# Kernel optimization log

Hardware: AMD Instinct MI355X
Metric: run time of the kernel (lower is better)

Reference implementation:

```python
import jax, jax.numpy as jnp
import numpy as np

B, N, E = 4, 2048, 1024          # batch, seq, embed_dim
H = 8                            # num_heads
D1 = 3 * E                       # expand_ratio * embed_dim = 3072 (already divisible by H)
DH = D1 // H                     # head_dim = 384
R = 512                          # rpe_embedding
GAMMA = 0.99
EPS = 1e-8


def _srms(x):
    # SimpleRMSNorm: x / (||x||_2 * d^{-1/2} + eps), no learned params
    rms = jnp.linalg.norm(x, axis=-1, keepdims=True) * (x.shape[-1] ** -0.5)
    return x / (rms + EPS)


def setup_inputs() -> dict:
    key = jax.random.key(0)
    ks = jax.random.split(key, 20)

    def lin(k, din, dout):
        kw, kb = jax.random.split(k)
        w = jax.random.normal(kw, (din, dout), jnp.float32) * (din ** -0.5)
        b = jax.random.normal(kb, (dout,), jnp.float32) * 0.02
        return w, b

    x = jax.random.normal(ks[0], (B, N, E), jnp.float32)
    u_w, u_b = lin(ks[1], E, D1)
    v_w, v_b = lin(ks[2], E, D1)
    o_w, o_b = lin(ks[3], D1, E)
    pos_w, pos_b = lin(ks[4], 1, R)
    lw0, lb0 = lin(ks[5], R, R)
    lw1, lb1 = lin(ks[6], R, R)
    lw2, lb2 = lin(ks[7], R, R)
    out_w, out_b = lin(ks[8], R, H * DH)
    return dict(x=x, u_w=u_w, u_b=u_b, v_w=v_w, v_b=v_b, o_w=o_w, o_b=o_b,
                pos_w=pos_w, pos_b=pos_b, lw0=lw0, lb0=lb0, lw1=lw1, lb1=lb1,
                lw2=lw2, lb2=lb2, out_w=out_w, out_b=out_b)


def reference(x, u_w, u_b, v_w, v_b, o_w, o_b,
              pos_w, pos_b, lw0, lb0, lw1, lb1, lw2, lb2, out_w, out_b):
    b, n, _ = x.shape
    # gated projections
    u = jax.nn.silu(x @ u_w + u_b)                       # (b, n, d1)
    v = jax.nn.silu(x @ v_w + v_b)                       # (b, n, d1)
    v = v.reshape(b, n, H, DH).transpose(0, 2, 1, 3)     # (b, h, n, d)

    # --- Tno: RPE MLP produces Toeplitz coefficients for lags 0..n-1 ---
    pos_idx = jnp.arange(n, dtype=x.dtype)[:, None]      # (n, 1)
    h_ = pos_idx @ pos_w + pos_b                         # (n, R)
    for w, bb in ((lw0, lb0), (lw1, lb1), (lw2, lb2)):
        h_ = jax.nn.relu(_srms(h_)) @ w + bb             # non-residual rpe layers
    coefs = jax.nn.relu(_srms(h_)) @ out_w + out_b       # (n, h*d)
    coefs = coefs.reshape(n, H, DH).transpose(1, 0, 2)   # (h, n, d)

    zero = coefs[:, :1]                                  # lag 0
    pos = coefs[:, 1:]                                   # lags 1..n-1
    decay = GAMMA ** jnp.arange(1, n, dtype=x.dtype)[None, :, None]
    pos = pos * decay                                    # use_decay with fixed gamma buffer
    # causal: negative lags are zero; cat([zero, pos, zero]) then zero-pad to 2n
    a = jnp.concatenate([zero, pos, zero], axis=1)       # (h, n+1, d)

    # circular conv of length 2n == causal Toeplitz matmul
    m = 2 * n
    av = jnp.fft.rfft(a, m, axis=1)                      # (h, m//2+1, d)
    xv = jnp.fft.rfft(v, m, axis=2)                      # (b, h, m//2+1, d)
    tv = jnp.fft.irfft(av[None] * xv, m, axis=2)[:, :, :n, :]

    out = tv.transpose(0, 2, 1, 3).reshape(b, n, H * DH) # (b, n, d1)
    out = u * out                                        # gate
    return out @ o_w + o_b                               # (b, n, e)
```

## Files before the change

### kernel.cpp

```cpp
#include <hip/hip_runtime.h>
#include <hip/hip_bf16.h>
#include <math.h>

#define GAMMA_ 0.99f
#define EPS_ 1e-8f

typedef __attribute__((ext_vector_type(8))) short s16x8;
typedef __attribute__((ext_vector_type(4))) float f32x4;
typedef __attribute__((address_space(1))) const ushort GASu;
typedef __attribute__((address_space(3))) ushort LASu;

__device__ __forceinline__ unsigned short f2bf(float f){
  unsigned u = __float_as_uint(f);
  unsigned r = (u + 0x7FFFu + ((u >> 16) & 1u)) >> 16;
  return (unsigned short)r;
}
__device__ __forceinline__ float bf2f(unsigned short h){
  return __uint_as_float(((unsigned)h) << 16);
}

__device__ __forceinline__ float2 cmul(float2 a, float2 b){
  return make_float2(a.x*b.x - a.y*b.y, a.x*b.y + a.y*b.x);
}
__device__ __forceinline__ float2 cadd(float2 a, float2 b){ return make_float2(a.x+b.x, a.y+b.y); }
__device__ __forceinline__ float2 csub(float2 a, float2 b){ return make_float2(a.x-b.x, a.y-b.y); }

__device__ void fft_dif(float2* z, const float2* tw, int tid){
  for (int s = 0; s < 12; ++s){
    __syncthreads();
    int half = 2048 >> s;
    for (int b = tid; b < 2048; b += 256){
      int j  = b & (half - 1);
      int g  = b >> (11 - s);
      int i0 = (g << (12 - s)) + j;
      int i1 = i0 + half;
      float2 u = z[i0], v = z[i1];
      z[i0] = cadd(u, v);
      z[i1] = cmul(csub(u, v), tw[j << s]);
    }
  }
  __syncthreads();
}
__device__ void fft_dit(float2* z, const float2* tw, int tid){
  for (int s = 0; s < 12; ++s){
    __syncthreads();
    int half = 1 << s;
    for (int b = tid; b < 2048; b += 256){
      int j  = b & (half - 1);
      int g  = b >> s;
      int i0 = (g << (s + 1)) + j;
      int i1 = i0 + half;
      float2 u = z[i0];
      float2 t = cmul(z[i1], tw[j << (11 - s)]);
      z[i0] = cadd(u, t);
      z[i1] = csub(u, t);
    }
  }
  __syncthreads();
}
__device__ __forceinline__ void tw_init(float2* tw, int tid){
  for (int j = tid; j < 2048; j += 256){
    float th = -(float)(3.14159265358979323846 / 2048.0) * (float)j;
    float s_, c_; __sincosf(th, &s_, &c_);
    tw[j] = make_float2(c_, s_);
  }
}
__device__ __forceinline__ int rev12(int x){ return (int)(__brev((unsigned)x) >> 20); }

__global__ __launch_bounds__(256)
void transpose_split(const float* __restrict__ W, ushort* __restrict__ Th,
                     ushort* __restrict__ Tl, int K, int N){
  __shared__ float T[32][33];
  int n0 = blockIdx.x * 32, k0 = blockIdx.y * 32;
  int tid = threadIdx.x;
  int j = tid & 31, i = tid >> 5;
#pragma unroll
  for (int p = 0; p < 4; ++p)
    T[i + 8*p][j] = W[(size_t)(k0 + i + 8*p) * N + n0 + j];
  __syncthreads();
#pragma unroll
  for (int p = 0; p < 4; ++p){
    int r = i + 8*p;
    float f = T[j][r];
    unsigned short hh = f2bf(f);
    Th[(size_t)(n0 + r) * K + k0 + j] = hh;
    Tl[(size_t)(n0 + r) * K + k0 + j] = f2bf(f - bf2f(hh));
  }
}

template<int ACT, int OUTMODE, int ASRC>
__global__ __launch_bounds__(256)
void gemm_mfma(const float* __restrict__ Af,
               const ushort* __restrict__ Ah, const ushort* __restrict__ Al,
               const ushort* __restrict__ Bh, const ushort* __restrict__ Bl,
               const float* __restrict__ bias,
               float* __restrict__ C, ushort* __restrict__ Ch, ushort* __restrict__ Cl,
               int M, int N, int K)
{
  __shared__ ushort Ash[128*32];
  __shared__ ushort Asl[128*32];
  __shared__ ushort Bsh[128*32];
  __shared__ ushort Bsl[128*32];
  int tid = threadIdx.x;
  int gx = gridDim.x;
  int nwg = gx * gridDim.y;
  int flat = blockIdx.y * gx + blockIdx.x;
  int s = (flat & 7) * (nwg >> 3) + (flat >> 3);
  int bx = s % gx, by = s / gx;
  int row0 = by * 128, col0 = bx * 128;
  int w = tid >> 6, lane = tid & 63;
  int wm = w >> 1, wn = w & 1;
  int lr = lane & 15, lg = lane >> 4;
  f32x4 acc[4][4] = {};

  for (int k0 = 0; k0 < K; k0 += 32){
    __syncthreads();
#pragma unroll
    for (int i = 0; i < 2; ++i){
      int p   = (w << 7) + (i << 6) + lane;
      int r   = p >> 2, chp = p & 3;
      int ch  = chp ^ ((r >> 1) & 3);
      int lbase = (w << 10) + (i << 9);
      size_t gb = (size_t)(col0 + r) * K + k0 + (ch << 3);
      __builtin_amdgcn_global_load_lds((GASu*)(Bh + gb), (LASu*)(Bsh + lbase), 16, 0, 0);
      __builtin_amdgcn_global_load_lds((GASu*)(Bl + gb), (LASu*)(Bsl + lbase), 16, 0, 0);
      if (ASRC == 0){
        size_t ga = (size_t)(row0 + r) * K + k0 + (ch << 3);
        __builtin_amdgcn_global_load_lds((GASu*)(Ah + ga), (LASu*)(Ash + lbase), 16, 0, 0);
        __builtin_amdgcn_global_load_lds((GASu*)(Al + ga), (LASu*)(Asl + lbase), 16, 0, 0);
      }
    }
    if (ASRC == 1){
#pragma unroll
      for (int pp = 0; pp < 2; ++pp){
        int c = tid + (pp << 8);
        int r = c >> 2, ch = c & 3;
        int kk = ch << 3;
        int off = (r << 5) + ((ch ^ ((r >> 1) & 3)) << 3);
        const float* src = &Af[(size_t)(row0 + r) * K + k0 + kk];
        float4 f0 = *(const float4*)src;
        float4 f1 = *(const float4*)(src + 4);
        float fs[8] = {f0.x, f0.y, f0.z, f0.w, f1.x, f1.y, f1.z, f1.w};
        uint hv[4], lv[4];
#pragma unroll
        for (int q = 0; q < 4; ++q){
          unsigned short h0 = f2bf(fs[2*q]),     h1 = f2bf(fs[2*q+1]);
          unsigned short l0 = f2bf(fs[2*q]   - bf2f(h0));
          unsigned short l1 = f2bf(fs[2*q+1] - bf2f(h1));
          hv[q] = (uint)h0 | ((uint)h1 << 16);
          lv[q] = (uint)l0 | ((uint)l1 << 16);
        }
        *(uint4*)&Ash[off] = make_uint4(hv[0], hv[1], hv[2], hv[3]);
        *(uint4*)&Asl[off] = make_uint4(lv[0], lv[1], lv[2], lv[3]);
      }
    }
    __syncthreads();
    s16x8 ah[4], al[4], bh[4], bl[4];
#pragma unroll
    for (int m = 0; m < 4; ++m){
      int row = wm*64 + m*16 + lr;
      int aoff = (row << 5) + ((lg ^ ((row >> 1) & 3)) << 3);
      ah[m] = *(const s16x8*)&Ash[aoff];
      al[m] = *(const s16x8*)&Asl[aoff];
    }
#pragma unroll
    for (int n = 0; n < 4; ++n){
      int row = wn*64 + n*16 + lr;
      int boff = (row << 5) + ((lg ^ ((row >> 1) & 3)) << 3);
      bh[n] = *(const s16x8*)&Bsh[boff];
      bl[n] = *(const s16x8*)&Bsl[boff];
    }
#pragma unroll
    for (int m = 0; m < 4; ++m)
#pragma unroll
      for (int n = 0; n < 4; ++n){
        acc[m][n] = __builtin_amdgcn_mfma_f32_16x16x32_bf16(ah[m], bh[n], acc[m][n], 0, 0, 0);
        acc[m][n] = __builtin_amdgcn_mfma_f32_16x16x32_bf16(ah[m], bl[n], acc[m][n], 0, 0, 0);
        acc[m][n] = __builtin_amdgcn_mfma_f32_16x16x32_bf16(al[m], bh[n], acc[m][n], 0, 0, 0);
      }
  }

#pragma unroll
  for (int m = 0; m < 4; ++m){
    int grow_base = row0 + wm*64 + m*16 + lg*4;
#pragma unroll
    for (int n = 0; n < 4; ++n){
      int gcol = col0 + wn*64 + n*16 + lr;
      float bv = bias[gcol];
      if (OUTMODE == 1){
        float4 o; float* op = (float*)&o;
#pragma unroll
        for (int r = 0; r < 4; ++r){
          float v2 = acc[m][n][r] + bv;
          if (ACT) v2 = v2 / (1.f + __expf(-v2));
          op[r] = v2;
        }
        int bb = grow_base >> 11, t = grow_base & 2047;
        *(float4*)&C[((size_t)bb * N + gcol) * 2048 + t] = o;
      } else {
#pragma unroll
        for (int r = 0; r < 4; ++r){
          float v2 = acc[m][n][r] + bv;
          if (ACT) v2 = v2 / (1.f + __expf(-v2));
          int grow = grow_base + r;
          if (OUTMODE == 0){
            C[(size_t)grow * N + gcol] = v2;
          } else {
            unsigned short hh = f2bf(v2);
            Ch[(size_t)grow * N + gcol] = hh;
            Cl[(size_t)grow * N + gcol] = f2bf(v2 - bf2f(hh));
          }
        }
      }
    }
  }
}

__global__ __launch_bounds__(256)
void pos_init(const float* __restrict__ pw, const float* __restrict__ pb, float* __restrict__ h){
  int idx = blockIdx.x * 256 + threadIdx.x;
  int t = idx >> 9, r = idx & 511;
  h[idx] = (float)t * pw[r] + pb[r];
}

__global__ __launch_bounds__(256)
void srms_relu_split(const float* __restrict__ in, ushort* __restrict__ oh,
                     ushort* __restrict__ ol){
  __shared__ float red[256];
  int row = blockIdx.x, tid = threadIdx.x;
  const float* r = in + (size_t)row * 512;
  float a = r[tid], b = r[tid + 256];
  red[tid] = a*a + b*b;
  __syncthreads();
  for (int off = 128; off > 0; off >>= 1){
    if (tid < off) red[tid] += red[tid + off];
    __syncthreads();
  }
  float rms = sqrtf(red[0] * (1.f / 512.f));
  float inv = 1.f / (rms + EPS_);
  size_t base = (size_t)row * 512;
  float va = a * inv; va = va > 0.f ? va : 0.f;
  float vb = b * inv; vb = vb > 0.f ? vb : 0.f;
  unsigned short ha = f2bf(va), hb = f2bf(vb);
  oh[base + tid]       = ha; ol[base + tid]       = f2bf(va - bf2f(ha));
  oh[base + tid + 256] = hb; ol[base + tid + 256] = f2bf(vb - bf2f(hb));
}

__global__ __launch_bounds__(256)
void build_aspec(const float* __restrict__ coefs_t, float2* __restrict__ aspec, int pbase){
  __shared__ float2 z[4096];
  __shared__ float2 tw[2048];
  int tid = threadIdx.x, slot = blockIdx.x, p = pbase + slot;
  tw_init(tw, tid);
  const float* c0 = coefs_t + (size_t)(2*p) * 2048;
  const float* c1 = c0 + 2048;
  const float l2g = log2f(GAMMA_);
  for (int t = tid; t < 2048; t += 256){
    float g = exp2f(l2g * (float)t);
    z[t] = make_float2(c0[t] * g, c1[t] * g);
  }
  for (int t = 2048 + tid; t < 4096; t += 256) z[t] = make_float2(0.f, 0.f);
  fft_dif(z, tw, tid);
  for (int k = tid; k <= 2048; k += 256){
    float2 zk = z[rev12(k)];
    float2 zm = z[rev12((4096 - k) & 4095)];
    float2 A0 = make_float2(0.5f*(zk.x + zm.x),  0.5f*(zk.y - zm.y));
    float2 A1 = make_float2(0.5f*(zk.y + zm.y), -0.5f*(zk.x - zm.x));
    *(float4*)(aspec + ((size_t)slot * 2049 + k) * 2) = make_float4(A0.x, A0.y, A1.x, A1.y);
  }
}

__global__ __launch_bounds__(256)
void conv_fft(float* __restrict__ vt, const float4* __restrict__ aspec, int pbase){
  __shared__ float2 z[4096];
  __shared__ float2 tw[2048];
  int tid = threadIdx.x, slot = blockIdx.x, p = pbase + slot, bb = blockIdx.y;
  tw_init(tw, tid);
  float* v0 = vt + ((size_t)bb * 3072 + 2*p) * 2048;
  float* v1 = v0 + 2048;
  for (int t = tid; t < 2048; t += 256) z[t] = make_float2(v0[t], v1[t]);
  for (int t = 2048 + tid; t < 4096; t += 256) z[t] = make_float2(0.f, 0.f);
  fft_dif(z, tw, tid);
  for (int k = tid; k <= 2048; k += 256){
    int rk  = rev12(k);
    int rmk = rev12((4096 - k) & 4095);
    float2 zk = z[rk], zm = z[rmk];
    float2 V0 = make_float2(0.5f*(zk.x + zm.x),  0.5f*(zk.y - zm.y));
    float2 V1 = make_float2(0.5f*(zk.y + zm.y), -0.5f*(zk.x - zm.x));
    float4 av = aspec[(size_t)slot * 2049 + k];
    float2 P0 = cmul(V0, make_float2(av.x, av.y));
    float2 P1 = cmul(V1, make_float2(av.z, av.w));
    z[rk]  = make_float2(P0.x - P1.y, -(P0.y + P1.x));
    z[rmk] = make_float2(P0.x + P1.y,   P0.y - P1.x);
  }
  fft_dit(z, tw, tid);
  const float sc = 1.f / 4096.f;
  for (int t = tid; t < 2048; t += 256){
    float2 w = z[t];
    v0[t] =  w.x * sc;
    v1[t] = -w.y * sc;
  }
}

__global__ __launch_bounds__(256)
void fuse_mul_inplace(ushort* uh, ushort* ul, const float* __restrict__ vt){
  __shared__ float T[64][65];
  int tid = threadIdx.x;
  int c0 = blockIdx.x * 64, t0 = blockIdx.y * 64;
  size_t b = blockIdx.z;
  {
    int j = tid >> 2, q = tid & 3;
    const float* src = vt + ((b * 3072 + c0 + j) * 2048 + t0 + q * 16);
#pragma unroll
    for (int f = 0; f < 4; ++f){
      float4 v = *(const float4*)(src + f * 4);
      T[j][q*16 + f*4 + 0] = v.x;
      T[j][q*16 + f*4 + 1] = v.y;
      T[j][q*16 + f*4 + 2] = v.z;
      T[j][q*16 + f*4 + 3] = v.w;
    }
  }
  __syncthreads();
  int i = tid >> 3, jq = tid & 7;
#pragma unroll
  for (int f = 0; f < 2; ++f){
    int row = i + f*32;
    size_t base = ((size_t)b * 2048 + t0 + row) * 3072 + c0 + jq*8;
    uint4 hv = *(const uint4*)&uh[base];
    uint4 lv = *(const uint4*)&ul[base];
    const uint* hp = (const uint*)&hv;
    const uint* lp = (const uint*)&lv;
    uint hr[4], lw[4];
#pragma unroll
    for (int e = 0; e < 4; ++e){
      int ch0 = jq*8 + e*2;
      float u0 = bf2f((unsigned short)(hp[e] & 0xffffu)) + bf2f((unsigned short)(lp[e] & 0xffffu));
      float u1 = bf2f((unsigned short)(hp[e] >> 16))     + bf2f((unsigned short)(lp[e] >> 16));
      float p0 = u0 * T[ch0][row];
      float p1 = u1 * T[ch0 + 1][row];
      unsigned short h0 = f2bf(p0), l0 = f2bf(p0 - bf2f(h0));
      unsigned short h1 = f2bf(p1), l1 = f2bf(p1 - bf2f(h1));
      hr[e] = (uint)h0 | ((uint)h1 << 16);
      lw[e] = (uint)l0 | ((uint)l1 << 16);
    }
    *(uint4*)&uh[base] = make_uint4(hr[0], hr[1], hr[2], hr[3]);
    *(uint4*)&ul[base] = make_uint4(lw[0], lw[1], lw[2], lw[3]);
  }
}

extern "C" void kernel_launch(void* const* d_in, const int* in_sizes, int n_in,
                              void* d_out, int out_size, void* d_ws, size_t ws_size,
                              hipStream_t stream)
{
  const float* x     = (const float*)d_in[0];
  const float* u_w   = (const float*)d_in[1];
  const float* u_b   = (const float*)d_in[2];
  const float* v_w   = (const float*)d_in[3];
  const float* v_b   = (const float*)d_in[4];
  const float* o_w   = (const float*)d_in[5];
  const float* o_b   = (const float*)d_in[6];
  const float* pos_w = (const float*)d_in[7];
  const float* pos_b = (const float*)d_in[8];
  const float* lw0   = (const float*)d_in[9];
  const float* lb0   = (const float*)d_in[10];
  const float* lw1   = (const float*)d_in[11];
  const float* lb1   = (const float*)d_in[12];
  const float* lw2   = (const float*)d_in[13];
  const float* lb2   = (const float*)d_in[14];
  const float* out_w = (const float*)d_in[15];
  const float* out_b = (const float*)d_in[16];
  float* out = (float*)d_out;

  if (ws_size < 219152384) return;

  char* ws = (char*)d_ws;
  ushort* uhi  = (ushort*)(ws);
  ushort* ulo  = (ushort*)(ws + 50331648);
  float*  vt   = (float*) (ws + 100663296);
  char* R = ws + 201326592;
  ushort* wT_h   = (ushort*)(R);
  ushort* wT_l   = (ushort*)(R + 6291456);
  ushort* hb_h   = (ushort*)(R);
  ushort* hb_l   = (ushort*)(R + 2097152);
  ushort* owtT_h = (ushort*)(R + 4194304);
  ushort* owtT_l = (ushort*)(R + 7340032);
  float*  h_a    = (float*) (R + 10485760);
  ushort* lw0T_h = (ushort*)(R + 14680064);
  ushort* lw0T_l = (ushort*)(R + 15204352);
  ushort* lw1T_h = (ushort*)(R + 15728640);
  ushort* lw1T_l = (ushort*)(R + 16252928);
  ushort* lw2T_h = (ushort*)(R + 16777216);
  ushort* lw2T_l = (ushort*)(R + 17301504);
  float*  coefs_t= (float*)d_out;
  float2* aspec  = (float2*)(R);
  ushort* owT_h  = (ushort*)(R);
  ushort* owT_l  = (ushort*)(R + 6291456);

  dim3 blk(256);
  transpose_split<<<dim3(96, 32), blk, 0, stream>>>(u_w, wT_h, wT_l, 1024, 3072);
  gemm_mfma<1,2,1><<<dim3(24, 64), blk, 0, stream>>>(x, nullptr, nullptr, wT_h, wT_l, u_b,
                                                     nullptr, uhi, ulo, 8192, 3072, 1024);
  transpose_split<<<dim3(96, 32), blk, 0, stream>>>(v_w, wT_h, wT_l, 1024, 3072);
  gemm_mfma<1,1,1><<<dim3(24, 64), blk, 0, stream>>>(x, nullptr, nullptr, wT_h, wT_l, v_b,
                                                     vt, nullptr, nullptr, 8192, 3072, 1024);
  pos_init<<<4096, blk, 0, stream>>>(pos_w, pos_b, h_a);
  transpose_split<<<dim3(16, 16), blk, 0, stream>>>(lw0, lw0T_h, lw0T_l, 512, 512);
  transpose_split<<<dim3(16, 16), blk, 0, stream>>>(lw1, lw1T_h, lw1T_l, 512, 512);
  transpose_split<<<dim3(16, 16), blk, 0, stream>>>(lw2, lw2T_h, lw2T_l, 512, 512);
  transpose_split<<<dim3(96, 16), blk, 0, stream>>>(out_w, owtT_h, owtT_l, 512, 3072);
  srms_relu_split<<<2048, blk, 0, stream>>>(h_a, hb_h, hb_l);
  gemm_mfma<0,0,0><<<dim3(4, 16), blk, 0, stream>>>(nullptr, hb_h, hb_l, lw0T_h, lw0T_l, lb0,
                                                    h_a, nullptr, nullptr, 2048, 512, 512);
  srms_relu_split<<<2048, blk, 0, stream>>>(h_a, hb_h, hb_l);
  gemm_mfma<0,0,0><<<dim3(4, 16), blk, 0, stream>>>(nullptr, hb_h, hb_l, lw1T_h, lw1T_l, lb1,
                                                    h_a, nullptr, nullptr, 2048, 512, 512);
  srms_relu_split<<<2048, blk, 0, stream>>>(h_a, hb_h, hb_l);
  gemm_mfma<0,0,0><<<dim3(4, 16), blk, 0, stream>>>(nullptr, hb_h, hb_l, lw2T_h, lw2T_l, lb2,
                                                    h_a, nullptr, nullptr, 2048, 512, 512);
  srms_relu_split<<<2048, blk, 0, stream>>>(h_a, hb_h, hb_l);
  gemm_mfma<0,1,0><<<dim3(24, 16), blk, 0, stream>>>(nullptr, hb_h, hb_l, owtT_h, owtT_l, out_b,
                                                     coefs_t, nullptr, nullptr, 2048, 3072, 512);
  for (int pass = 0; pass < 6; ++pass){
    build_aspec<<<256, blk, 0, stream>>>(coefs_t, aspec, pass * 256);
    conv_fft<<<dim3(256, 4), blk, 0, stream>>>(vt, (const float4*)aspec, pass * 256);
  }
  transpose_split<<<dim3(32, 96), blk, 0, stream>>>(o_w, owT_h, owT_l, 3072, 1024);
  fuse_mul_inplace<<<dim3(48, 32, 4), blk, 0, stream>>>(uhi, ulo, vt);
  gemm_mfma<0,0,0><<<dim3(8, 64), blk, 0, stream>>>(nullptr, uhi, ulo, owT_h, owT_l, o_b,
                                                    out, nullptr, nullptr, 8192, 1024, 3072);
}
```

Measured before the change: 1.276 ms.

## Fuse kernel spectrum build into FFT convolution, keeping spectrum in registers

Replaces the six passes of build_aspec plus conv_fft launches with one kernel of 1536 blocks. Each block computes the Toeplitz kernel spectrum for a head-dim pair, holds it in registers, then loops over the 4 batches doing forward FFT, pointwise multiply and inverse FFT. This drops the global aspec buffer round-trip and 11 launches. In exchange each block does four times more serial work, has fewer blocks in flight, and uses more registers for the 36 held spectrum values.

```diff
diff --git a/kernel.cpp b/kernel.cpp
--- a/kernel.cpp
+++ b/kernel.cpp
@@ -247,58 +247,66 @@
 }
 
 __global__ __launch_bounds__(256)
-void build_aspec(const float* __restrict__ coefs_t, float2* __restrict__ aspec, int pbase){
+void conv_fft_all(float* __restrict__ vt, const float* __restrict__ coefs_t){
   __shared__ float2 z[4096];
   __shared__ float2 tw[2048];
-  int tid = threadIdx.x, slot = blockIdx.x, p = pbase + slot;
+  int tid = threadIdx.x, p = blockIdx.x;
   tw_init(tw, tid);
-  const float* c0 = coefs_t + (size_t)(2*p) * 2048;
-  const float* c1 = c0 + 2048;
-  const float l2g = log2f(GAMMA_);
-  for (int t = tid; t < 2048; t += 256){
-    float g = exp2f(l2g * (float)t);
-    z[t] = make_float2(c0[t] * g, c1[t] * g);
-  }
-  for (int t = 2048 + tid; t < 4096; t += 256) z[t] = make_float2(0.f, 0.f);
+  {
+    const float* c0 = coefs_t + (size_t)(2*p) * 2048;
+    const float* c1 = c0 + 2048;
+    const float l2g = log2f(GAMMA_);
+    for (int t = tid; t < 2048; t += 256){
+      float g = exp2f(l2g * (float)t);
+      z[t] = make_float2(c0[t] * g, c1[t] * g);
+    }
+    for (int t = 2048 + tid; t < 4096; t += 256) z[t] = make_float2(0.f, 0.f);
+  }
   fft_dif(z, tw, tid);
-  for (int k = tid; k <= 2048; k += 256){
-    float2 zk = z[rev12(k)];
-    float2 zm = z[rev12((4096 - k) & 4095)];
-    float2 A0 = make_float2(0.5f*(zk.x + zm.x),  0.5f*(zk.y - zm.y));
-    float2 A1 = make_float2(0.5f*(zk.y + zm.y), -0.5f*(zk.x - zm.x));
-    *(float4*)(aspec + ((size_t)slot * 2049 + k) * 2) = make_float4(A0.x, A0.y, A1.x, A1.y);
-  }
-}
-
-__global__ __launch_bounds__(256)
-void conv_fft(float* __restrict__ vt, const float4* __restrict__ aspec, int pbase){
-  __shared__ float2 z[4096];
-  __shared__ float2 tw[2048];
-  int tid = threadIdx.x, slot = blockIdx.x, p = pbase + slot, bb = blockIdx.y;
-  tw_init(tw, tid);
-  float* v0 = vt + ((size_t)bb * 3072 + 2*p) * 2048;
-  float* v1 = v0 + 2048;
-  for (int t = tid; t < 2048; t += 256) z[t] = make_float2(v0[t], v1[t]);
-  for (int t = 2048 + tid; t < 4096; t += 256) z[t] = make_float2(0.f, 0.f);
-  fft_dif(z, tw, tid);
-  for (int k = tid; k <= 2048; k += 256){
-    int rk  = rev12(k);
-    int rmk = rev12((4096 - k) & 4095);
-    float2 zk = z[rk], zm = z[rmk];
-    float2 V0 = make_float2(0.5f*(zk.x + zm.x),  0.5f*(zk.y - zm.y));
-    float2 V1 = make_float2(0.5f*(zk.y + zm.y), -0.5f*(zk.x - zm.x));
-    float4 av = aspec[(size_t)slot * 2049 + k];
-    float2 P0 = cmul(V0, make_float2(av.x, av.y));
-    float2 P1 = cmul(V1, make_float2(av.z, av.w));
-    z[rk]  = make_float2(P0.x - P1.y, -(P0.y + P1.x));
-    z[rmk] = make_float2(P0.x + P1.y,   P0.y - P1.x);
-  }
-  fft_dit(z, tw, tid);
-  const float sc = 1.f / 4096.f;
-  for (int t = tid; t < 2048; t += 256){
-    float2 w = z[t];
-    v0[t] =  w.x * sc;
-    v1[t] = -w.y * sc;
+  float2 a0r[9], a1r[9];
+#pragma unroll 9
+  for (int j = 0; j < 9; ++j){
+    int k = tid + (j << 8);
+    if (k <= 2048){
+      float2 zk = z[rev12(k)];
+      float2 zm = z[rev12((4096 - k) & 4095)];
+      a0r[j] = make_float2(0.5f*(zk.x + zm.x),  0.5f*(zk.y - zm.y));
+      a1r[j] = make_float2(0.5f*(zk.y + zm.y), -0.5f*(zk.x - zm.x));
+    } else {
+      a0r[j] = make_float2(0.f, 0.f);
+      a1r[j] = make_float2(0.f, 0.f);
+    }
+  }
+  __syncthreads();
+  for (int bb = 0; bb < 4; ++bb){
+    float* v0 = vt + ((size_t)bb * 3072 + 2*p) * 2048;
+    float* v1 = v0 + 2048;
+    for (int t = tid; t < 2048; t += 256) z[t] = make_float2(v0[t], v1[t]);
+    for (int t = 2048 + tid; t < 4096; t += 256) z[t] = make_float2(0.f, 0.f);
+    fft_dif(z, tw, tid);
+#pragma unroll 9
+    for (int j = 0; j < 9; ++j){
+      int k = tid + (j << 8);
+      if (k <= 2048){
+        int rk  = rev12(k);
+        int rmk = rev12((4096 - k) & 4095);
+        float2 zk = z[rk], zm = z[rmk];
+        float2 V0 = make_float2(0.5f*(zk.x + zm.x),  0.5f*(zk.y - zm.y));
+        float2 V1 = make_float2(0.5f*(zk.y + zm.y), -0.5f*(zk.x - zm.x));
+        float2 P0 = cmul(V0, a0r[j]);
+        float2 P1 = cmul(V1, a1r[j]);
+        z[rk]  = make_float2(P0.x - P1.y, -(P0.y + P1.x));
+        z[rmk] = make_float2(P0.x + P1.y,   P0.y - P1.x);
+      }
+    }
+    fft_dit(z, tw, tid);
+    const float sc = 1.f / 4096.f;
+    for (int t = tid; t < 2048; t += 256){
+      float2 w = z[t];
+      v0[t] =  w.x * sc;
+      v1[t] = -w.y * sc;
+    }
+    __syncthreads();
   }
 }
 
@@ -392,7 +400,6 @@
   ushort* lw2T_h = (ushort*)(R + 16777216);
   ushort* lw2T_l = (ushort*)(R + 17301504);
   float*  coefs_t= (float*)d_out;
-  float2* aspec  = (float2*)(R);
   ushort* owT_h  = (ushort*)(R);
   ushort* owT_l  = (ushort*)(R + 6291456);
 
@@ -420,10 +427,7 @@
   srms_relu_split<<<2048, blk, 0, stream>>>(h_a, hb_h, hb_l);
   gemm_mfma<0,1,0><<<dim3(24, 16), blk, 0, stream>>>(nullptr, hb_h, hb_l, owtT_h, owtT_l, out_b,
                                                      coefs_t, nullptr, nullptr, 2048, 3072, 512);
-  for (int pass = 0; pass < 6; ++pass){
-    build_aspec<<<256, blk, 0, stream>>>(coefs_t, aspec, pass * 256);
-    conv_fft<<<dim3(256, 4), blk, 0, stream>>>(vt, (const float4*)aspec, pass * 256);
-  }
+  conv_fft_all<<<1536, blk, 0, stream>>>(vt, coefs_t);
   transpose_split<<<dim3(32, 96), blk, 0, stream>>>(o_w, owT_h, owT_l, 3072, 1024);
   fuse_mul_inplace<<<dim3(48, 32, 4), blk, 0, stream>>>(uhi, ulo, vt);
   gemm_mfma<0,0,0><<<dim3(8, 64), blk, 0, stream>>>(nullptr, uhi, ulo, owT_h, owT_l, o_b,
```

After: 1.226 ms. 3.9% less time.
